# Kernel tuning notes

Hardware: AMD Instinct MI355X
Metric: run time of the kernel (lower is better)

Reference implementation:

```python
import jax, jax.numpy as jnp
import numpy as np

EMB = 1024
HEADS = 16
HEAD_DIM = EMB // HEADS
EPS = 1e-5


def gelu_tanh(x):
    c = jnp.sqrt(jnp.asarray(2.0 / jnp.pi, x.dtype))
    return 0.5 * x * (1 + jnp.tanh(c * (x + 0.044715 * x ** 3)))


def layernorm(x, scale, shift):
    mean = jnp.mean(x, axis=-1, keepdims=True)
    var = jnp.mean((x - mean) ** 2, axis=-1, keepdims=True)
    return scale * (x - mean) / jnp.sqrt(var + EPS) + shift


def setup_inputs() -> dict:
    key = jax.random.key(0)
    ks = jax.random.split(key, 12)
    s = 0.02
    x = jax.random.normal(ks[0], (2, 2048, EMB), dtype=jnp.float32)
    Wq = jax.random.normal(ks[1], (EMB, EMB), dtype=jnp.float32) * s
    Wk = jax.random.normal(ks[2], (EMB, EMB), dtype=jnp.float32) * s
    Wv = jax.random.normal(ks[3], (EMB, EMB), dtype=jnp.float32) * s
    Wo = jax.random.normal(ks[4], (EMB, EMB), dtype=jnp.float32) * s
    bo = jnp.zeros((EMB,), jnp.float32)
    W1 = jax.random.normal(ks[5], (EMB, 4 * EMB), dtype=jnp.float32) * s
    b1 = jnp.zeros((4 * EMB,), jnp.float32)
    W2 = jax.random.normal(ks[6], (4 * EMB, EMB), dtype=jnp.float32) * s
    b2 = jnp.zeros((EMB,), jnp.float32)
    g1 = jnp.ones((EMB,), jnp.float32)
    s1 = jnp.zeros((EMB,), jnp.float32)
    g2 = jnp.ones((EMB,), jnp.float32)
    s2 = jnp.zeros((EMB,), jnp.float32)
    return {"x": x, "Wq": Wq, "Wk": Wk, "Wv": Wv, "Wo": Wo, "bo": bo,
            "W1": W1, "b1": b1, "W2": W2, "b2": b2,
            "g1": g1, "s1": s1, "g2": g2, "s2": s2}


def reference(x, Wq, Wk, Wv, Wo, bo, W1, b1, W2, b2, g1, s1, g2, s2):
    B, S, D = x.shape
    # --- attention sub-block (pre-LN) ---
    h = layernorm(x, g1, s1)
    q = (h @ Wq).reshape(B, S, HEADS, HEAD_DIM).transpose(0, 2, 1, 3)
    k = (h @ Wk).reshape(B, S, HEADS, HEAD_DIM).transpose(0, 2, 1, 3)
    v = (h @ Wv).reshape(B, S, HEADS, HEAD_DIM).transpose(0, 2, 1, 3)
    scores = jnp.einsum('bhqd,bhkd->bhqk', q, k) / jnp.sqrt(
        jnp.asarray(HEAD_DIM, x.dtype))
    causal = jnp.triu(jnp.ones((S, S), bool), k=1)
    scores = jnp.where(causal, -jnp.inf, scores)
    attn = jax.nn.softmax(scores, axis=-1)
    ctx = jnp.einsum('bhqk,bhkd->bhqd', attn, v)
    ctx = ctx.transpose(0, 2, 1, 3).reshape(B, S, D)
    x = x + (ctx @ Wo + bo)
    # --- FFN sub-block (pre-LN) ---
    h = layernorm(x, g2, s2)
    h = gelu_tanh(h @ W1 + b1) @ W2 + b2
    return x + h
```

## Files before the change

### kernel.cpp

```cpp
#include <hip/hip_runtime.h>
#include <hip/hip_bf16.h>
#include <math.h>
#include <stdint.h>

typedef __bf16 bf16;
typedef __bf16 bf16x2 __attribute__((ext_vector_type(2)));
typedef __bf16 bf16x4 __attribute__((ext_vector_type(4)));
typedef __bf16 bf16x8 __attribute__((ext_vector_type(8)));
typedef float f32x4 __attribute__((ext_vector_type(4)));
typedef float f32x16 __attribute__((ext_vector_type(16)));
typedef unsigned uint2v __attribute__((ext_vector_type(2)));
typedef unsigned uint4v __attribute__((ext_vector_type(4)));

#define MFMA16(a, b, c) __builtin_amdgcn_mfma_f32_16x16x32_bf16((a), (b), (c), 0, 0, 0)
#define MFMA32(a, b, c) __builtin_amdgcn_mfma_f32_32x32x16_bf16((a), (b), (c), 0, 0, 0)

constexpr int EMB = 1024;
constexpr int SEQ = 2048;
constexpr int BATCH = 2;
constexpr int NTOK = BATCH * SEQ;
constexpr int FFN = 4 * EMB;
constexpr int HEADS = 16;
constexpr int HDIM = 64;

#define QSCALE 0.18033688011112042f

__device__ __forceinline__ void gload16(const void* g, void* l) {
    __builtin_amdgcn_global_load_lds(
        (const __attribute__((address_space(1))) void*)g,
        (__attribute__((address_space(3))) void*)l,
        16, 0, 0);
}

__device__ __forceinline__ float xhalf_max(float x) {
    unsigned u = __float_as_uint(x);
    uint2v r = __builtin_amdgcn_permlane32_swap(u, u, false, false);
    return fmaxf(__uint_as_float(r[0]), __uint_as_float(r[1]));
}
__device__ __forceinline__ float xhalf_sum(float x) {
    unsigned u = __float_as_uint(x);
    uint2v r = __builtin_amdgcn_permlane32_swap(u, u, false, false);
    return __uint_as_float(r[0]) + __uint_as_float(r[1]);
}

__device__ __forceinline__ unsigned pkbf(float a, float b) {
    bf16x2 v;
    v[0] = (bf16)a;
    v[1] = (bf16)b;
    return __builtin_bit_cast(unsigned, v);
}

__device__ __forceinline__ float gelu_f(float u) {
    float w_ = 0.7978845608028654f * (u + 0.044715f * u * u * u);
    float z = __builtin_amdgcn_exp2f(-2.8853900817779268f * w_);
    return u / (1.f + z);
}

__global__ __launch_bounds__(256) void ln_kernel(const float* __restrict__ x,
                                                 const float* __restrict__ g,
                                                 const float* __restrict__ b,
                                                 bf16* __restrict__ out) {
    int row = blockIdx.x;
    int t = threadIdx.x;
    float4 v = reinterpret_cast<const float4*>(x + (size_t)row * EMB)[t];
    float s = v.x + v.y + v.z + v.w;
    float s2 = v.x * v.x + v.y * v.y + v.z * v.z + v.w * v.w;
#pragma unroll
    for (int o = 1; o < 64; o <<= 1) {
        s += __shfl_xor(s, o);
        s2 += __shfl_xor(s2, o);
    }
    __shared__ float ps[4], ps2[4];
    int w = t >> 6;
    if ((t & 63) == 0) { ps[w] = s; ps2[w] = s2; }
    __syncthreads();
    s = ps[0] + ps[1] + ps[2] + ps[3];
    s2 = ps2[0] + ps2[1] + ps2[2] + ps2[3];
    float mean = s * (1.f / EMB);
    float var = s2 * (1.f / EMB) - mean * mean;
    float rstd = rsqrtf(var + 1e-5f);
    float4 gv = reinterpret_cast<const float4*>(g)[t];
    float4 bv = reinterpret_cast<const float4*>(b)[t];
    bf16* op = out + (size_t)row * EMB + t * 4;
    op[0] = (bf16)(gv.x * (v.x - mean) * rstd + bv.x);
    op[1] = (bf16)(gv.y * (v.y - mean) * rstd + bv.y);
    op[2] = (bf16)(gv.z * (v.z - mean) * rstd + bv.z);
    op[3] = (bf16)(gv.w * (v.w - mean) * rstd + bv.w);
}

__global__ __launch_bounds__(256) void transpose_all(
    const float* __restrict__ Wq, const float* __restrict__ Wk,
    const float* __restrict__ Wv, const float* __restrict__ Wo,
    const float* __restrict__ W1, const float* __restrict__ W2,
    bf16* __restrict__ Wqkvt, bf16* __restrict__ Wot,
    bf16* __restrict__ W1t, bf16* __restrict__ W2t) {
    int b = blockIdx.x;
    const float* W;
    bf16* Wt;
    int K, N, tile;
    if (b < 4096) {
        int w = b >> 10;
        tile = b & 1023;
        W = (w == 0) ? Wq : (w == 1) ? Wk : (w == 2) ? Wv : Wo;
        Wt = (w == 3) ? Wot : Wqkvt + (size_t)w * EMB * EMB;
        K = EMB; N = EMB;
    } else if (b < 8192) {
        tile = b - 4096; W = W1; Wt = W1t; K = EMB; N = FFN;
    } else {
        tile = b - 8192; W = W2; Wt = W2t; K = FFN; N = EMB;
    }
    int ntx = N / 32;
    int n0 = (tile % ntx) * 32, k0 = (tile / ntx) * 32;
    __shared__ float tl[32][33];
    int tx = threadIdx.x & 31, ty = threadIdx.x >> 5;
#pragma unroll
    for (int i = 0; i < 4; i++)
        tl[ty + 8 * i][tx] = W[(size_t)(k0 + ty + 8 * i) * N + n0 + tx];
    __syncthreads();
#pragma unroll
    for (int i = 0; i < 4; i++)
        Wt[(size_t)(n0 + ty + 8 * i) * K + k0 + tx] = (bf16)tl[tx][ty + 8 * i];
}

__global__ __launch_bounds__(256) void vtrans(const bf16* __restrict__ v,
                                              bf16* __restrict__ vt) {
    int bh = blockIdx.y;
    int s0 = blockIdx.x * 64;
    const bf16* src = v + (size_t)bh * SEQ * HDIM + (size_t)s0 * HDIM;
    bf16* dst = vt + (size_t)bh * HDIM * SEQ + s0;
    __shared__ bf16 tile[64][72];
    int t = threadIdx.x;
    int s = t >> 2, d0 = (t & 3) * 16;
    bf16x8 a = *reinterpret_cast<const bf16x8*>(src + s * HDIM + d0);
    bf16x8 b = *reinterpret_cast<const bf16x8*>(src + s * HDIM + d0 + 8);
#pragma unroll
    for (int e = 0; e < 8; e++) {
        tile[d0 + e][s] = a[e];
        tile[d0 + 8 + e][s] = b[e];
    }
    __syncthreads();
    int d = t >> 2, c0 = (t & 3) * 16;
    bf16x8 o0 = *reinterpret_cast<const bf16x8*>(&tile[d][c0]);
    bf16x8 o1 = *reinterpret_cast<const bf16x8*>(&tile[d][c0 + 8]);
    *reinterpret_cast<bf16x8*>(dst + (size_t)d * SEQ + c0) = o0;
    *reinterpret_cast<bf16x8*>(dst + (size_t)d * SEQ + c0 + 8) = o1;
}

template <int MODE>
__global__ __launch_bounds__(512, 1) void gemm8p(const bf16* __restrict__ A,
                                                 const bf16* __restrict__ Bt,
                                                 int K, int N,
                                                 bf16* __restrict__ outB,
                                                 bf16* __restrict__ outB2,
                                                 const float* __restrict__ bias) {
    extern __shared__ char smem[];
    int t = threadIdx.x;
    int wave = t >> 6, lane = t & 63;
    int wr = wave >> 2, wc = wave & 3;
    int lr = lane & 15, lg = lane >> 4;
    int row0 = blockIdx.x * 256;
    int col0 = blockIdx.y * 256;

    int tilesAll = K / 64;
    int nz = gridDim.z, z = blockIdx.z;
    int base = tilesAll / nz, rem = tilesAll - base * nz;
    int myT = base + (z < rem ? 1 : 0);
    int tBeg = z * base + (z < rem ? z : rem);

    const char* aSrc[4];
    const char* bSrc[4];
#pragma unroll
    for (int i = 0; i < 4; i++) {
        int f = t + i * 512;
        int gr = f >> 3, gk = f & 7;
        aSrc[i] = (const char*)A + ((size_t)(row0 + gr) * K + ((gk ^ (gr & 7)) << 3)) * 2
                  + (size_t)tBeg * 128;
        bSrc[i] = (const char*)Bt + ((size_t)(col0 + gr) * K + ((gk ^ (gr & 7)) << 3)) * 2
                  + (size_t)tBeg * 128;
    }

    f32x4 acc[8][4];
#pragma unroll
    for (int m = 0; m < 8; m++)
#pragma unroll
        for (int n = 0; n < 4; n++) acc[m][n] = f32x4{0.f, 0.f, 0.f, 0.f};

    gload16(bSrc[0], smem + 32768 + (t + 0 * 512) * 16);
    gload16(bSrc[1], smem + 32768 + (t + 1 * 512) * 16);
    gload16(bSrc[2], smem + 32768 + (t + 2 * 512) * 16);
    gload16(bSrc[3], smem + 32768 + (t + 3 * 512) * 16);
    gload16(aSrc[0], smem + (t + 0 * 512) * 16);
    gload16(aSrc[2], smem + (t + 2 * 512) * 16);
    gload16(aSrc[1], smem + (t + 1 * 512) * 16);
    gload16(aSrc[3], smem + (t + 3 * 512) * 16);
    asm volatile("s_waitcnt vmcnt(2)" ::: "memory");
    __builtin_amdgcn_s_barrier();

    for (int tk = 0; tk < myT; tk++) {
        int cur = tk & 1;
        const char* la = smem + cur * 65536;
        const char* lb = la + 32768;
        char* na = smem + (cur ^ 1) * 65536;
        bool stage = (tk + 1 < myT);

        bf16x8 bfr[2][4];
#pragma unroll
        for (int ph = 0; ph < 4; ph++) {
            constexpr int PH_KH[4] = {0, 0, 1, 1};
            constexpr int PH_MH[4] = {0, 1, 0, 1};
            const int kh = PH_KH[ph], mh = PH_MH[ph];
            bf16x8 afr[4];
#pragma unroll
            for (int m = 0; m < 4; m++) {
                int row = wr * 128 + (mh * 4 + m) * 16 + lr;
                int gk = kh * 4 + lg;
                afr[m] = *reinterpret_cast<const bf16x8*>(
                    la + row * 128 + ((gk ^ (row & 7)) << 4));
            }
            if (mh == 0) {
#pragma unroll
                for (int n = 0; n < 4; n++) {
                    int row = wc * 64 + n * 16 + lr;
                    int gk = kh * 4 + lg;
                    bfr[kh][n] = *reinterpret_cast<const bf16x8*>(
                        lb + row * 128 + ((gk ^ (row & 7)) << 4));
                }
            }
            if (stage) {
                if (ph == 0) {
                    gload16(bSrc[0] + 128, na + 32768 + (t + 0 * 512) * 16);
                    gload16(bSrc[1] + 128, na + 32768 + (t + 1 * 512) * 16);
                } else if (ph == 1) {
                    gload16(bSrc[2] + 128, na + 32768 + (t + 2 * 512) * 16);
                    gload16(bSrc[3] + 128, na + 32768 + (t + 3 * 512) * 16);
                } else if (ph == 2) {
                    gload16(aSrc[0] + 128, na + (t + 0 * 512) * 16);
                    gload16(aSrc[2] + 128, na + (t + 2 * 512) * 16);
                } else {
                    gload16(aSrc[1] + 128, na + (t + 1 * 512) * 16);
                    gload16(aSrc[3] + 128, na + (t + 3 * 512) * 16);
                }
            }
            __builtin_amdgcn_s_barrier();
            __builtin_amdgcn_s_setprio(1);
#pragma unroll
            for (int m = 0; m < 4; m++)
#pragma unroll
                for (int n = 0; n < 4; n++)
                    acc[mh * 4 + m][n] = MFMA16(afr[m], bfr[kh][n], acc[mh * 4 + m][n]);
            __builtin_amdgcn_s_setprio(0);
            if (ph == 0 || ph == 3)
                asm volatile("s_waitcnt vmcnt(2)" ::: "memory");
            __builtin_amdgcn_s_barrier();
        }
#pragma unroll
        for (int i = 0; i < 4; i++) { aSrc[i] += 128; bSrc[i] += 128; }
    }

    float bi[4];
    if (MODE == 2) {
#pragma unroll
        for (int n = 0; n < 4; n++) bi[n] = bias[col0 + wc * 64 + n * 16 + lr];
    }
    bf16* pd = outB;
    if (MODE == 3) pd = (z < 2) ? outB + (size_t)z * ((size_t)NTOK * EMB) : outB2;
#pragma unroll
    for (int mf = 0; mf < 8; mf++) {
#pragma unroll
        for (int r = 0; r < 4; r++) {
            int row = row0 + wr * 128 + mf * 16 + 4 * lg + r;
#pragma unroll
            for (int n = 0; n < 4; n++) {
                int col = col0 + wc * 64 + n * 16 + lr;
                float v = acc[mf][n][r];
                if (MODE == 0) {
                    int b_ = row >> 11, s_ = row & 2047;
                    int which = col >> 10, rem_ = col & 1023;
                    int h_ = rem_ >> 6, d_ = rem_ & 63;
                    float sc = (which == 0) ? QSCALE : 1.0f;
                    outB[(size_t)which * (NTOK * EMB) +
                         (((size_t)(b_ * HEADS + h_) * SEQ + s_) << 6) + d_] =
                        (bf16)(v * sc);
                } else if (MODE == 2) {
                    outB[(size_t)row * N + col] = (bf16)gelu_f(v + bi[n]);
                } else {
                    pd[(size_t)row * N + col] = (bf16)v;
                }
            }
        }
    }
}

__global__ __launch_bounds__(256) void ffn2_reduce(const float* __restrict__ x1,
                                                   const bf16* __restrict__ p01,
                                                   const bf16* __restrict__ p2,
                                                   const float* __restrict__ bias,
                                                   float* __restrict__ out) {
    constexpr int UNITS = NTOK * EMB / 4;
    const bf16* p1 = p01 + (size_t)NTOK * EMB;
    for (int i = blockIdx.x * 256 + threadIdx.x; i < UNITS; i += gridDim.x * 256) {
        float4 r = reinterpret_cast<const float4*>(x1)[i];
        float4 bv = reinterpret_cast<const float4*>(bias)[i & (EMB / 4 - 1)];
        bf16x4 a0 = reinterpret_cast<const bf16x4*>(p01)[i];
        bf16x4 a1 = reinterpret_cast<const bf16x4*>(p1)[i];
        bf16x4 a2 = reinterpret_cast<const bf16x4*>(p2)[i];
        r.x += (float)a0[0] + (float)a1[0] + (float)a2[0] + bv.x;
        r.y += (float)a0[1] + (float)a1[1] + (float)a2[1] + bv.y;
        r.z += (float)a0[2] + (float)a1[2] + (float)a2[2] + bv.z;
        r.w += (float)a0[3] + (float)a1[3] + (float)a2[3] + bv.w;
        reinterpret_cast<float4*>(out)[i] = r;
    }
}

template <int BM, int BN, int BK, int MODE>
__global__ __launch_bounds__(256) void gemm_lds(const bf16* __restrict__ A,
                                                const bf16* __restrict__ Bt,
                                                int M, int N, int K,
                                                float* __restrict__ outF,
                                                bf16* __restrict__ outB,
                                                const float* __restrict__ bias,
                                                const float* __restrict__ resid) {
    constexpr int MR = BM / 32;
    constexpr int NR = BN / 32;
    constexpr int ACH = (BM * BK * 2) / 4096;
    constexpr int BCH = (BN * BK * 2) / 4096;
    __shared__ bf16 sA[BM * BK];
    __shared__ bf16 sB[BN * BK];
    int t = threadIdx.x;
    int wave = t >> 6, lane = t & 63;
    int wr = wave >> 1, wc = wave & 1;
    int lr = lane & 15, lg = lane >> 4;
    int row0 = blockIdx.x * BM;
    int col0 = blockIdx.y * BN;

    const char* aS[ACH];
    const char* bS[BCH];
#pragma unroll
    for (int c = 0; c < ACH; c++) {
        int o = (t + c * 256) * 16;
        aS[c] = (const char*)A + (size_t)(row0 + o / (2 * BK)) * K * 2 + (o & (2 * BK - 1));
    }
#pragma unroll
    for (int c = 0; c < BCH; c++) {
        int o = (t + c * 256) * 16;
        bS[c] = (const char*)Bt + (size_t)(col0 + o / (2 * BK)) * K * 2 + (o & (2 * BK - 1));
    }

    f32x4 acc[MR][NR];
#pragma unroll
    for (int m = 0; m < MR; m++)
#pragma unroll
        for (int n = 0; n < NR; n++) acc[m][n] = f32x4{0.f, 0.f, 0.f, 0.f};

    for (int k0 = 0; k0 < K; k0 += BK) {
        __syncthreads();
#pragma unroll
        for (int c = 0; c < ACH; c++)
            gload16(aS[c], (char*)sA + (t + c * 256) * 16);
#pragma unroll
        for (int c = 0; c < BCH; c++)
            gload16(bS[c], (char*)sB + (t + c * 256) * 16);
#pragma unroll
        for (int c = 0; c < ACH; c++) aS[c] += 2 * BK;
#pragma unroll
        for (int c = 0; c < BCH; c++) bS[c] += 2 * BK;
        __syncthreads();

#pragma unroll
        for (int ks = 0; ks < BK / 32; ks++) {
            bf16x8 a[MR], b[NR];
#pragma unroll
            for (int m = 0; m < MR; m++)
                a[m] = *reinterpret_cast<const bf16x8*>(
                    sA + (wr * (BM / 2) + m * 16 + lr) * BK + ks * 32 + 8 * lg);
#pragma unroll
            for (int n = 0; n < NR; n++)
                b[n] = *reinterpret_cast<const bf16x8*>(
                    sB + (wc * (BN / 2) + n * 16 + lr) * BK + ks * 32 + 8 * lg);
#pragma unroll
            for (int m = 0; m < MR; m++)
#pragma unroll
                for (int n = 0; n < NR; n++)
                    acc[m][n] = MFMA16(a[m], b[n], acc[m][n]);
        }
    }

#pragma unroll
    for (int m = 0; m < MR; m++) {
#pragma unroll
        for (int r = 0; r < 4; r++) {
            int row = row0 + wr * (BM / 2) + m * 16 + 4 * lg + r;
#pragma unroll
            for (int n = 0; n < NR; n++) {
                int col = col0 + wc * (BN / 2) + n * 16 + lr;
                float v = acc[m][n][r];
                size_t idx = (size_t)row * N + col;
                outF[idx] = resid[idx] + v + bias[col];
            }
        }
    }
}

__global__ __launch_bounds__(256, 3) void attn_kernel(const bf16* __restrict__ q,
                                                      const bf16* __restrict__ k,
                                                      const bf16* __restrict__ vt,
                                                      bf16* __restrict__ ctx) {
    int wg = blockIdx.x;
    int wgid = (wg & 7) * 64 + (wg >> 3);
    int bh = wgid >> 4;
    int pair = wgid & 15;
    const bf16* qh = q + (size_t)bh * SEQ * HDIM;
    const bf16* kh = k + (size_t)bh * SEQ * HDIM;
    const bf16* vh = vt + (size_t)bh * HDIM * SEQ;
    int t = threadIdx.x;
    int wave = t >> 6, lane = t & 63;
    int ql = lane & 31, hi = lane >> 5;

    int span = (wave < 2 ? (31 - pair) : pair) * 64;
    int qrow = span + (wave & 1) * 32;
    int myNc = span / 64 + 1;
    int ncAll = 32 - pair;

    __shared__ bf16 sK[2][64 * 64];
    __shared__ bf16 sV[2][64 * 64];

    int grow = t >> 3, gg = t & 7;
    const bf16* kSrc0 = kh + (size_t)grow * HDIM + ((gg ^ (grow & 7)) << 3);
    const bf16* kSrc1 = kh + (size_t)(grow + 32) * HDIM + ((gg ^ ((grow + 32) & 7)) << 3);
    const bf16* vSrc0 = vh + (size_t)grow * SEQ + ((gg ^ (grow & 7)) << 3);
    const bf16* vSrc1 = vh + (size_t)(grow + 32) * SEQ + ((gg ^ ((grow + 32) & 7)) << 3);
    char* kD0 = (char*)&sK[0][0] + wave * 1024;
    char* vD0 = (char*)&sV[0][0] + wave * 1024;

    int b_ = bh >> 4, h_ = bh & 15;

    bf16x8 qf[4];
#pragma unroll
    for (int ks = 0; ks < 4; ks++)
        qf[ks] = *reinterpret_cast<const bf16x8*>(
            qh + (size_t)(qrow + ql) * HDIM + ks * 16 + 8 * hi);

    f32x16 o0, o1;
#pragma unroll
    for (int r = 0; r < 16; r++) { o0[r] = 0.f; o1[r] = 0.f; }
    float mx = -1e30f, lsum = 0.f;

    gload16(kSrc0, kD0);
    gload16(kSrc1, kD0 + 4096);
    gload16(vSrc0, vD0);
    gload16(vSrc1, vD0 + 4096);
    __syncthreads();

    for (int c = 0; c < ncAll; c++) {
        int c0 = c * 64;
        if (c + 1 < ncAll) {
            int nb = (c + 1) & 1;
            int cn = c0 + 64;
            gload16(kSrc0 + (size_t)cn * HDIM, kD0 + nb * 8192);
            gload16(kSrc1 + (size_t)cn * HDIM, kD0 + nb * 8192 + 4096);
            gload16(vSrc0 + cn, vD0 + nb * 8192);
            gload16(vSrc1 + cn, vD0 + nb * 8192 + 4096);
        }

        if (c < myNc) {
            const char* kb_ = (const char*)&sK[c & 1][0];
            const char* vb_ = (const char*)&sV[c & 1][0];

            f32x16 st0, st1;
#pragma unroll
            for (int r = 0; r < 16; r++) { st0[r] = 0.f; st1[r] = 0.f; }
#pragma unroll
            for (int ks = 0; ks < 4; ks++) {
                int so = ((2 * ks + hi) ^ (ql & 7)) << 4;
                bf16x8 kA0 = *reinterpret_cast<const bf16x8*>(kb_ + ql * 128 + so);
                bf16x8 kA1 = *reinterpret_cast<const bf16x8*>(kb_ + (32 + ql) * 128 + so);
                st0 = MFMA32(kA0, qf[ks], st0);
                st1 = MFMA32(kA1, qf[ks], st1);
            }

            if (c == myNc - 1) {
#pragma unroll
                for (int r = 0; r < 16; r++) {
                    int kl = c0 + (r & 3) + 8 * (r >> 2) + 4 * hi;
                    if (kl > qrow + ql) st0[r] = -1e30f;
                    if (kl + 32 > qrow + ql) st1[r] = -1e30f;
                }
            }

            float pmax = -1e30f;
#pragma unroll
            for (int r = 0; r < 16; r++)
                pmax = fmaxf(pmax, fmaxf(st0[r], st1[r]));
            pmax = xhalf_max(pmax);
            float mxold = mx;
            bool defer = (pmax <= mxold + 8.0f);
            float mn = defer ? mxold : fmaxf(mxold, pmax);
            mx = mn;
            float ps = 0.f;
#pragma unroll
            for (int r = 0; r < 16; r++) {
                st0[r] = __builtin_amdgcn_exp2f(st0[r] - mn);
                st1[r] = __builtin_amdgcn_exp2f(st1[r] - mn);
                ps += st0[r] + st1[r];
            }
            ps = xhalf_sum(ps);
            if (!__all(defer)) {
                float scl = __builtin_amdgcn_exp2f(mxold - mn);
                lsum = lsum * scl + ps;
#pragma unroll
                for (int r = 0; r < 16; r++) { o0[r] *= scl; o1[r] *= scl; }
            } else {
                lsum += ps;
            }

#pragma unroll
            for (int h2 = 0; h2 < 2; h2++) {
                f32x16 P = h2 ? st1 : st0;
#pragma unroll
                for (int sub = 0; sub < 2; sub++) {
                    int ks = 2 * h2 + sub;
                    int bs = 8 * sub;
                    unsigned X0 = pkbf(P[bs + 0], P[bs + 1]);
                    unsigned X1 = pkbf(P[bs + 2], P[bs + 3]);
                    unsigned Y0 = pkbf(P[bs + 4], P[bs + 5]);
                    unsigned Y1 = pkbf(P[bs + 6], P[bs + 7]);
                    uint2v s0 = __builtin_amdgcn_permlane32_swap(X0, Y0, false, false);
                    uint2v s1 = __builtin_amdgcn_permlane32_swap(X1, Y1, false, false);
                    uint4v uw;
                    uw[0] = s0[0];
                    uw[1] = s1[0];
                    uw[2] = s0[1];
                    uw[3] = s1[1];
                    bf16x8 pb = __builtin_bit_cast(bf16x8, uw);
                    int so = ((2 * ks + hi) ^ (ql & 7)) << 4;
                    bf16x8 vA0 = *reinterpret_cast<const bf16x8*>(vb_ + ql * 128 + so);
                    bf16x8 vA1 = *reinterpret_cast<const bf16x8*>(vb_ + (32 + ql) * 128 + so);
                    o0 = MFMA32(vA0, pb, o0);
                    o1 = MFMA32(vA1, pb, o1);
                }
            }
        }

        __syncthreads();
    }

    float inv = 1.f / lsum;
    size_t base = ((size_t)b_ * SEQ + qrow + ql) * EMB + h_ * HDIM;
#pragma unroll
    for (int j = 0; j < 4; j++) {
        bf16x4 w0, w1;
#pragma unroll
        for (int e = 0; e < 4; e++) {
            w0[e] = (bf16)(o0[4 * j + e] * inv);
            w1[e] = (bf16)(o1[4 * j + e] * inv);
        }
        *reinterpret_cast<bf16x4*>(ctx + base + 8 * j + 4 * hi) = w0;
        *reinterpret_cast<bf16x4*>(ctx + base + 32 + 8 * j + 4 * hi) = w1;
    }
}

extern "C" void kernel_launch(void* const* d_in, const int* in_sizes, int n_in,
                              void* d_out, int out_size, void* d_ws, size_t ws_size,
                              hipStream_t stream) {
    const float* x  = (const float*)d_in[0];
    const float* Wq = (const float*)d_in[1];
    const float* Wk = (const float*)d_in[2];
    const float* Wv = (const float*)d_in[3];
    const float* Wo = (const float*)d_in[4];
    const float* bo = (const float*)d_in[5];
    const float* W1 = (const float*)d_in[6];
    const float* b1 = (const float*)d_in[7];
    const float* W2 = (const float*)d_in[8];
    const float* b2 = (const float*)d_in[9];
    const float* g1 = (const float*)d_in[10];
    const float* s1 = (const float*)d_in[11];
    const float* g2 = (const float*)d_in[12];
    const float* s2 = (const float*)d_in[13];

    const size_t MB = 1ull << 20;
    char* w = (char*)d_ws;
    bf16* Wqkvt = (bf16*)(w + 0 * MB);
    bf16* Wot = (bf16*)(w + 6 * MB);
    bf16* W1t = (bf16*)(w + 8 * MB);
    bf16* W2t = (bf16*)(w + 16 * MB);
    bf16* hbuf = (bf16*)(w + 24 * MB);
    bf16* vtb  = (bf16*)(w + 24 * MB);
    bf16* qkvb = (bf16*)(w + 32 * MB);
    bf16* qb   = (bf16*)(w + 32 * MB);
    bf16* kb   = (bf16*)(w + 40 * MB);
    bf16* vb   = (bf16*)(w + 48 * MB);
    bf16* ctxb = (bf16*)(w + 56 * MB);
    bf16* midb = (bf16*)(w + 32 * MB);
    float* x1  = (float*)(w + 64 * MB);
    bf16* p01  = (bf16*)(w + 0 * MB);
    bf16* p2   = (bf16*)(w + 24 * MB);

    hipFuncSetAttribute(reinterpret_cast<const void*>(gemm8p<0>),
                        hipFuncAttributeMaxDynamicSharedMemorySize, 131072);
    hipFuncSetAttribute(reinterpret_cast<const void*>(gemm8p<2>),
                        hipFuncAttributeMaxDynamicSharedMemorySize, 131072);
    hipFuncSetAttribute(reinterpret_cast<const void*>(gemm8p<3>),
                        hipFuncAttributeMaxDynamicSharedMemorySize, 131072);

    transpose_all<<<dim3(12288), 256, 0, stream>>>(Wq, Wk, Wv, Wo, W1, W2,
                                                   Wqkvt, Wot, W1t, W2t);

    ln_kernel<<<NTOK, 256, 0, stream>>>(x, g1, s1, hbuf);

    gemm8p<0><<<dim3(NTOK / 256, 3072 / 256), 512, 131072, stream>>>(
        hbuf, Wqkvt, EMB, 3072, qkvb, nullptr, nullptr);

    vtrans<<<dim3(SEQ / 64, BATCH * HEADS), 256, 0, stream>>>(vb, vtb);

    attn_kernel<<<dim3(512), 256, 0, stream>>>(qb, kb, vtb, ctxb);

    gemm_lds<128, 64, 32, 1><<<dim3(NTOK / 128, EMB / 64), 256, 0, stream>>>(
        ctxb, Wot, NTOK, EMB, EMB, x1, nullptr, bo, x);

    ln_kernel<<<NTOK, 256, 0, stream>>>(x1, g2, s2, hbuf);

    gemm8p<2><<<dim3(NTOK / 256, FFN / 256), 512, 131072, stream>>>(
        hbuf, W1t, EMB, FFN, midb, nullptr, b1);

    gemm8p<3><<<dim3(NTOK / 256, EMB / 256, 3), 512, 131072, stream>>>(
        midb, W2t, FFN, EMB, p01, p2, nullptr);
    ffn2_reduce<<<dim3(2048), 256, 0, stream>>>(x1, p01, p2, b2, (float*)d_out);
}
```

Baseline: 233.1 us.

## Process 128-key tiles per attention iteration instead of 64

The causal attention kernel now stages and processes 128 keys per loop step (K tile 128x64, V split into two 64-column halves), with double-buffered LDS doubled accordingly. This halves the number of loop iterations, syncthreads barriers and online-softmax rescale passes, and gives more MFMAs per sync. It doubles LDS use and register pressure (four score accumulators), so occupancy is lowered from 3 to 2 blocks per CU, and the diagonal tile may now include more fully masked work.

```diff
diff --git a/kernel.cpp b/kernel.cpp
--- a/kernel.cpp
+++ b/kernel.cpp
@@ -401,7 +401,7 @@
     }
 }
 
-__global__ __launch_bounds__(256, 3) void attn_kernel(const bf16* __restrict__ q,
+__global__ __launch_bounds__(256, 2) void attn_kernel(const bf16* __restrict__ q,
                                                       const bf16* __restrict__ k,
                                                       const bf16* __restrict__ vt,
                                                       bf16* __restrict__ ctx) {
@@ -416,21 +416,25 @@
     int wave = t >> 6, lane = t & 63;
     int ql = lane & 31, hi = lane >> 5;
 
-    int span = (wave < 2 ? (31 - pair) : pair) * 64;
-    int qrow = span + (wave & 1) * 32;
-    int myNc = span / 64 + 1;
-    int ncAll = 32 - pair;
-
-    __shared__ bf16 sK[2][64 * 64];
-    __shared__ bf16 sV[2][64 * 64];
+    int s64 = (wave < 2) ? (31 - pair) : pair;
+    int qrow = s64 * 64 + (wave & 1) * 32;
+    int myNc = (s64 >> 1) + 1;
+    int ncAll = ((31 - pair) >> 1) + 1;
+
+    __shared__ bf16 sK[2][128 * 64];
+    __shared__ bf16 sV[2][2][64 * 64];
 
     int grow = t >> 3, gg = t & 7;
-    const bf16* kSrc0 = kh + (size_t)grow * HDIM + ((gg ^ (grow & 7)) << 3);
-    const bf16* kSrc1 = kh + (size_t)(grow + 32) * HDIM + ((gg ^ ((grow + 32) & 7)) << 3);
-    const bf16* vSrc0 = vh + (size_t)grow * SEQ + ((gg ^ (grow & 7)) << 3);
-    const bf16* vSrc1 = vh + (size_t)(grow + 32) * SEQ + ((gg ^ ((grow + 32) & 7)) << 3);
-    char* kD0 = (char*)&sK[0][0] + wave * 1024;
-    char* vD0 = (char*)&sV[0][0] + wave * 1024;
+    const bf16* kS[4];
+#pragma unroll
+    for (int i = 0; i < 4; i++)
+        kS[i] = kh + (size_t)(grow + 32 * i) * HDIM + ((gg ^ ((grow + 32 * i) & 7)) << 3);
+    const bf16* vS[2];
+#pragma unroll
+    for (int i = 0; i < 2; i++)
+        vS[i] = vh + (size_t)(grow + 32 * i) * SEQ + ((gg ^ ((grow + 32 * i) & 7)) << 3);
+    char* kD = (char*)&sK[0][0] + wave * 1024;
+    char* vD = (char*)&sV[0][0][0] + wave * 1024;
 
     int b_ = bh >> 4, h_ = bh & 15;
 
@@ -445,52 +449,65 @@
     for (int r = 0; r < 16; r++) { o0[r] = 0.f; o1[r] = 0.f; }
     float mx = -1e30f, lsum = 0.f;
 
-    gload16(kSrc0, kD0);
-    gload16(kSrc1, kD0 + 4096);
-    gload16(vSrc0, vD0);
-    gload16(vSrc1, vD0 + 4096);
+#pragma unroll
+    for (int i = 0; i < 4; i++) gload16(kS[i], kD + i * 4096);
+#pragma unroll
+    for (int hh = 0; hh < 2; hh++)
+#pragma unroll
+        for (int i = 0; i < 2; i++)
+            gload16(vS[i] + 64 * hh, vD + hh * 8192 + i * 4096);
     __syncthreads();
 
     for (int c = 0; c < ncAll; c++) {
-        int c0 = c * 64;
+        int c0 = c * 128;
         if (c + 1 < ncAll) {
             int nb = (c + 1) & 1;
-            int cn = c0 + 64;
-            gload16(kSrc0 + (size_t)cn * HDIM, kD0 + nb * 8192);
-            gload16(kSrc1 + (size_t)cn * HDIM, kD0 + nb * 8192 + 4096);
-            gload16(vSrc0 + cn, vD0 + nb * 8192);
-            gload16(vSrc1 + cn, vD0 + nb * 8192 + 4096);
+            int cn = c0 + 128;
+#pragma unroll
+            for (int i = 0; i < 4; i++)
+                gload16(kS[i] + (size_t)cn * HDIM, kD + nb * 16384 + i * 4096);
+#pragma unroll
+            for (int hh = 0; hh < 2; hh++)
+#pragma unroll
+                for (int i = 0; i < 2; i++)
+                    gload16(vS[i] + cn + 64 * hh,
+                            vD + nb * 16384 + hh * 8192 + i * 4096);
         }
 
         if (c < myNc) {
             const char* kb_ = (const char*)&sK[c & 1][0];
-            const char* vb_ = (const char*)&sV[c & 1][0];
-
-            f32x16 st0, st1;
-#pragma unroll
-            for (int r = 0; r < 16; r++) { st0[r] = 0.f; st1[r] = 0.f; }
+
+            f32x16 st[4];
+#pragma unroll
+            for (int kg = 0; kg < 4; kg++)
+#pragma unroll
+                for (int r = 0; r < 16; r++) st[kg][r] = 0.f;
 #pragma unroll
             for (int ks = 0; ks < 4; ks++) {
                 int so = ((2 * ks + hi) ^ (ql & 7)) << 4;
-                bf16x8 kA0 = *reinterpret_cast<const bf16x8*>(kb_ + ql * 128 + so);
-                bf16x8 kA1 = *reinterpret_cast<const bf16x8*>(kb_ + (32 + ql) * 128 + so);
-                st0 = MFMA32(kA0, qf[ks], st0);
-                st1 = MFMA32(kA1, qf[ks], st1);
+#pragma unroll
+                for (int kg = 0; kg < 4; kg++) {
+                    bf16x8 kA = *reinterpret_cast<const bf16x8*>(
+                        kb_ + (kg * 32 + ql) * 128 + so);
+                    st[kg] = MFMA32(kA, qf[ks], st[kg]);
+                }
             }
 
             if (c == myNc - 1) {
 #pragma unroll
-                for (int r = 0; r < 16; r++) {
-                    int kl = c0 + (r & 3) + 8 * (r >> 2) + 4 * hi;
-                    if (kl > qrow + ql) st0[r] = -1e30f;
-                    if (kl + 32 > qrow + ql) st1[r] = -1e30f;
-                }
+                for (int kg = 0; kg < 4; kg++)
+#pragma unroll
+                    for (int r = 0; r < 16; r++) {
+                        int kl = c0 + kg * 32 + (r & 3) + 8 * (r >> 2) + 4 * hi;
+                        if (kl > qrow + ql) st[kg][r] = -1e30f;
+                    }
             }
 
             float pmax = -1e30f;
 #pragma unroll
-            for (int r = 0; r < 16; r++)
-                pmax = fmaxf(pmax, fmaxf(st0[r], st1[r]));
+            for (int kg = 0; kg < 4; kg++)
+#pragma unroll
+                for (int r = 0; r < 16; r++) pmax = fmaxf(pmax, st[kg][r]);
             pmax = xhalf_max(pmax);
             float mxold = mx;
             bool defer = (pmax <= mxold + 8.0f);
@@ -498,11 +515,12 @@
             mx = mn;
             float ps = 0.f;
 #pragma unroll
-            for (int r = 0; r < 16; r++) {
-                st0[r] = __builtin_amdgcn_exp2f(st0[r] - mn);
-                st1[r] = __builtin_amdgcn_exp2f(st1[r] - mn);
-                ps += st0[r] + st1[r];
-            }
+            for (int kg = 0; kg < 4; kg++)
+#pragma unroll
+                for (int r = 0; r < 16; r++) {
+                    st[kg][r] = __builtin_amdgcn_exp2f(st[kg][r] - mn);
+                    ps += st[kg][r];
+                }
             ps = xhalf_sum(ps);
             if (!__all(defer)) {
                 float scl = __builtin_amdgcn_exp2f(mxold - mn);
@@ -514,11 +532,11 @@
             }
 
 #pragma unroll
-            for (int h2 = 0; h2 < 2; h2++) {
-                f32x16 P = h2 ? st1 : st0;
+            for (int kg = 0; kg < 4; kg++) {
+                f32x16 P = st[kg];
 #pragma unroll
                 for (int sub = 0; sub < 2; sub++) {
-                    int ks = 2 * h2 + sub;
+                    int ks8 = 2 * kg + sub;
                     int bs = 8 * sub;
                     unsigned X0 = pkbf(P[bs + 0], P[bs + 1]);
                     unsigned X1 = pkbf(P[bs + 2], P[bs + 3]);
@@ -532,7 +550,9 @@
                     uw[2] = s0[1];
                     uw[3] = s1[1];
                     bf16x8 pb = __builtin_bit_cast(bf16x8, uw);
-                    int so = ((2 * ks + hi) ^ (ql & 7)) << 4;
+                    const char* vb_ = (const char*)&sV[c & 1][ks8 >> 2][0];
+                    int kss = ks8 & 3;
+                    int so = ((2 * kss + hi) ^ (ql & 7)) << 4;
                     bf16x8 vA0 = *reinterpret_cast<const bf16x8*>(vb_ + ql * 128 + so);
                     bf16x8 vA1 = *reinterpret_cast<const bf16x8*>(vb_ + (32 + ql) * 128 + so);
                     o0 = MFMA32(vA0, pb, o0);
```

Result: faster. 228.0 us (median of 2 runs) (-2.2%).
